# Kernel tuning notes

Hardware: AMD Instinct MI355X
Metric: run time of the kernel (lower is better)

## Reference

```python
import jax, jax.numpy as jnp
import numpy as np
import math

B, T, C = 1, 2048, 512
NH, NKV, HD, W = 8, 4, 64, 128  # heads, kv heads, head_dim, window_size
THETA = 10000.0
EPS = 1e-6


def _rms(x, w):
    # RMSNorm over last (head_dim) axis with learnable scale w
    return x * jax.lax.rsqrt(jnp.mean(x * x, axis=-1, keepdims=True) + EPS) * w


def _rope(x, cos, sin):
    # x: (B, H, T, HD); cos/sin: (T, HD//2). Half-split rotation.
    h = x.shape[-1] // 2
    x1, x2 = x[..., :h], x[..., h:]
    return jnp.concatenate([x1 * cos - x2 * sin, x2 * cos + x1 * sin], axis=-1)


def setup_inputs():
    key = jax.random.key(0)
    ks = jax.random.split(key, 5)
    x = jax.random.normal(ks[0], (B, T, C), jnp.float32)
    s = 1.0 / math.sqrt(C)
    W_q = jax.random.normal(ks[1], (C, NH * HD), jnp.float32) * s
    W_k = jax.random.normal(ks[2], (C, NKV * HD), jnp.float32) * s
    W_v = jax.random.normal(ks[3], (C, NKV * HD), jnp.float32) * s
    W_o = jax.random.normal(ks[4], (C, C), jnp.float32) * s
    q_norm_w = jnp.ones((HD,), jnp.float32)
    k_norm_w = jnp.ones((HD,), jnp.float32)
    pos = jnp.arange(T, dtype=jnp.float32)
    inv_freq = 1.0 / (THETA ** (jnp.arange(0, HD, 2, dtype=jnp.float32) / HD))
    ang = pos[:, None] * inv_freq[None, :]  # (T, HD//2)
    return {"x": x, "W_q": W_q, "W_k": W_k, "W_v": W_v, "W_o": W_o,
            "q_norm_w": q_norm_w, "k_norm_w": k_norm_w,
            "cos": jnp.cos(ang), "sin": jnp.sin(ang)}


def reference(x, W_q, W_k, W_v, W_o, q_norm_w, k_norm_w, cos, sin):
    q = (x @ W_q).reshape(B, T, NH, HD).transpose(0, 2, 1, 3)   # (B,NH,T,HD)
    k = (x @ W_k).reshape(B, T, NKV, HD).transpose(0, 2, 1, 3)  # (B,NKV,T,HD)
    v = (x @ W_v).reshape(B, T, NKV, HD).transpose(0, 2, 1, 3)
    q = _rope(q, cos, sin)
    k = _rope(k, cos, sin)
    q = _rms(q, q_norm_w)
    k = _rms(k, k_norm_w)
    g = NH // NKV  # GQA group size
    k = jnp.repeat(k, g, axis=1)  # (B,NH,T,HD)
    v = jnp.repeat(v, g, axis=1)
    # causal sliding-window: gather W-length windows ending at each position
    kp = jnp.pad(k, ((0, 0), (0, 0), (W - 1, 0), (0, 0)))
    vp = jnp.pad(v, ((0, 0), (0, 0), (W - 1, 0), (0, 0)))
    idx = jnp.arange(T)[:, None] + jnp.arange(W)[None, :]  # (T, W)
    kw = kp[:, :, idx, :]  # (B,NH,T,W,HD)
    vw = vp[:, :, idx, :]
    valid = jnp.arange(W)[None, :] >= (W - 1 - jnp.arange(T))[:, None]  # (T,W)
    attn = jnp.einsum('bhtd,bhtwd->bhtw', q, kw) / math.sqrt(HD)
    attn = jnp.where(valid[None, None], attn, -jnp.inf)
    attn = jax.nn.softmax(attn, axis=-1)
    out = jnp.einsum('bhtw,bhtwd->bhtd', attn, vw)  # (B,NH,T,HD)
    out = out.transpose(0, 2, 1, 3).reshape(B, T, C)
    return out @ W_o
```

## Files before the change

kernel.cpp:

```cpp
#include <hip/hip_runtime.h>
#include <hip/hip_bf16.h>
#include <math.h>

typedef float  f32x4  __attribute__((ext_vector_type(4)));
typedef short  s16x4  __attribute__((ext_vector_type(4)));
typedef short  s16x8  __attribute__((ext_vector_type(8)));
typedef unsigned short u16;

__device__ inline u16 f2b(float f) {
    __hip_bfloat16 h = __float2bfloat16(f);
    return *reinterpret_cast<u16*>(&h);
}
__device__ inline float b2f(u16 v) {
    return __uint_as_float(((unsigned)v) << 16);
}
__device__ inline void st_out(float* p, float v) { *p = v; }
__device__ inline void st_out(u16* p, float v)   { *p = f2b(v); }

__device__ inline void gload16(const void* g, void* l) {
    __builtin_amdgcn_global_load_lds(
        (const __attribute__((address_space(1))) void*)g,
        (__attribute__((address_space(3))) void*)l, 16, 0, 0);
}

__global__ __launch_bounds__(256) void prep(const float* __restrict__ x,
    const float* __restrict__ Wq, const float* __restrict__ Wk,
    const float* __restrict__ Wv, const float* __restrict__ Wo,
    u16* __restrict__ xb, u16* __restrict__ Wt, u16* __restrict__ Wot)
{
    const int tid = threadIdx.x, bid = blockIdx.x;
    if (bid >= 192) {
        int i = ((bid - 192) * 256 + tid) * 8;
        int row = i >> 9, col = i & 511;
        int scol = (col & ~63) | ((((col >> 3) & 7) ^ (row & 7)) << 3);
        float4 v0 = *(const float4*)(x + i);
        float4 v1 = *(const float4*)(x + i + 4);
        s16x8 o;
        o[0] = (short)f2b(v0.x); o[1] = (short)f2b(v0.y);
        o[2] = (short)f2b(v0.z); o[3] = (short)f2b(v0.w);
        o[4] = (short)f2b(v1.x); o[5] = (short)f2b(v1.y);
        o[6] = (short)f2b(v1.z); o[7] = (short)f2b(v1.w);
        *(s16x8*)(xb + (size_t)row * 512 + scol) = o;
        return;
    }
    __shared__ u16 Tsh[64][72];
    const float* src; u16* dst; int N, base, kt, nt;
    if (bid < 64)       { src = Wq; dst = Wt;  N = 512; base = 0;   kt = bid >> 3;       nt = bid & 7; }
    else if (bid < 96)  { src = Wk; dst = Wt;  N = 256; base = 512; kt = (bid-64) >> 2;  nt = (bid-64) & 3; }
    else if (bid < 128) { src = Wv; dst = Wt;  N = 256; base = 768; kt = (bid-96) >> 2;  nt = (bid-96) & 3; }
    else                { src = Wo; dst = Wot; N = 512; base = 0;   kt = (bid-128) >> 3; nt = (bid-128) & 7; }
    const int k0 = kt * 64, n0 = nt * 64;
    const int r = tid >> 2, c0 = (tid & 3) * 16;
#pragma unroll
    for (int j = 0; j < 4; ++j) {
        float4 v = *(const float4*)(src + (size_t)(k0 + r) * N + n0 + c0 + j * 4);
        Tsh[c0 + j*4 + 0][r] = f2b(v.x);
        Tsh[c0 + j*4 + 1][r] = f2b(v.y);
        Tsh[c0 + j*4 + 2][r] = f2b(v.z);
        Tsh[c0 + j*4 + 3][r] = f2b(v.w);
    }
    __syncthreads();
    const int n = tid >> 2, kc = (tid & 3) * 16;
    const int r7 = n & 7;
    const int cc0 = (kc >> 3) ^ r7;
    const int cc1 = ((kc >> 3) + 1) ^ r7;
    u16* oprow = dst + (size_t)(base + n0 + n) * 512 + k0;
    *(s16x8*)(oprow + cc0 * 8) = *(const s16x8*)&Tsh[n][kc];
    *(s16x8*)(oprow + cc1 * 8) = *(const s16x8*)&Tsh[n][kc + 8];
}

template<typename OutT>
__global__ __launch_bounds__(256) void gemm_mfma(const u16* __restrict__ A,
    const u16* __restrict__ Bt, OutT* __restrict__ C, int ldc)
{
    __shared__ u16 Ash[64][64];
    __shared__ u16 Bsh[64][64];
    const int tid = threadIdx.x;
    const int m0b = blockIdx.y * 64, n0b = blockIdx.x * 64;
    const int lane = tid & 63, wv = tid >> 6;
    const int q = lane & 15, g = lane >> 4;
    const int wm = (wv & 1) * 32, wn = (wv >> 1) * 32;
    const int lrow = lane >> 3, lchunk = lane & 7;
    const int s7 = q & 7;
    f32x4 acc[2][2] = {{{0,0,0,0},{0,0,0,0}},{{0,0,0,0},{0,0,0,0}}};
    for (int k0 = 0; k0 < 512; k0 += 64) {
        __syncthreads();
#pragma unroll
        for (int is = 0; is < 2; ++is) {
            const int rbase = is * 32 + wv * 8;
            gload16(A  + (size_t)(m0b + rbase + lrow) * 512 + k0 + lchunk * 8,
                    &Ash[rbase][0]);
            gload16(Bt + (size_t)(n0b + rbase + lrow) * 512 + k0 + lchunk * 8,
                    &Bsh[rbase][0]);
        }
        __syncthreads();
#pragma unroll
        for (int kk = 0; kk < 64; kk += 32) {
            const int cs = ((kk >> 3) + g) ^ s7;
            s16x8 af0 = *(const s16x8*)&Ash[wm + q][cs * 8];
            s16x8 af1 = *(const s16x8*)&Ash[wm + 16 + q][cs * 8];
            s16x8 bf0 = *(const s16x8*)&Bsh[wn + q][cs * 8];
            s16x8 bf1 = *(const s16x8*)&Bsh[wn + 16 + q][cs * 8];
            acc[0][0] = __builtin_amdgcn_mfma_f32_16x16x32_bf16(af0, bf0, acc[0][0], 0, 0, 0);
            acc[0][1] = __builtin_amdgcn_mfma_f32_16x16x32_bf16(af0, bf1, acc[0][1], 0, 0, 0);
            acc[1][0] = __builtin_amdgcn_mfma_f32_16x16x32_bf16(af1, bf0, acc[1][0], 0, 0, 0);
            acc[1][1] = __builtin_amdgcn_mfma_f32_16x16x32_bf16(af1, bf1, acc[1][1], 0, 0, 0);
        }
    }
#pragma unroll
    for (int mt = 0; mt < 2; ++mt)
#pragma unroll
        for (int nt = 0; nt < 2; ++nt)
#pragma unroll
            for (int r = 0; r < 4; ++r)
                st_out(&C[(size_t)(m0b + wm + mt*16 + g*4 + r) * ldc + n0b + wn + nt*16 + q],
                       acc[mt][nt][r]);
}

__global__ __launch_bounds__(256) void swa_mfma(const u16* __restrict__ qkvb,
    const float* __restrict__ cosT, const float* __restrict__ sinT,
    const float* __restrict__ qw, const float* __restrict__ kw,
    u16* __restrict__ attb)
{
    __shared__ u16 Ksh[160][72];
    __shared__ u16 Vt[64][162];
    const int tid = threadIdx.x;
    const int kvh = blockIdx.y;
    const int t0 = blockIdx.x * 32;
    for (int i = 0; i < 5; ++i) {
        int idx = i * 256 + tid;
        int j = idx >> 3, e = idx & 7, d0 = e * 8;
        int kt = t0 - 127 + j;
        if (kt < 0 || kt >= 2048) {
            s16x8 z = {0,0,0,0,0,0,0,0};
            *(s16x8*)&Ksh[j][d0] = z;
        } else {
            s16x8 raw = *(const s16x8*)(qkvb + (size_t)kt * 1024 + 512 + kvh * 64 + d0);
            float kv[8], ov[8];
#pragma unroll
            for (int ii = 0; ii < 8; ++ii) kv[ii] = b2f((u16)raw[ii]);
#pragma unroll
            for (int ii = 0; ii < 8; ++ii) ov[ii] = __shfl_xor(kv[ii], 4);
            const float* cp = cosT + kt * 32 + (e & 3) * 8;
            const float* sp = sinT + kt * 32 + (e & 3) * 8;
            float4 c0 = *(const float4*)(cp), c1 = *(const float4*)(cp + 4);
            float4 s0 = *(const float4*)(sp), s1 = *(const float4*)(sp + 4);
            float cf[8] = {c0.x,c0.y,c0.z,c0.w,c1.x,c1.y,c1.z,c1.w};
            float sf[8] = {s0.x,s0.y,s0.z,s0.w,s1.x,s1.y,s1.z,s1.w};
            const bool lo = (e < 4);
            float r[8]; float ssl = 0.f;
#pragma unroll
            for (int ii = 0; ii < 8; ++ii) {
                r[ii] = lo ? (kv[ii]*cf[ii] - ov[ii]*sf[ii])
                           : (kv[ii]*cf[ii] + ov[ii]*sf[ii]);
                ssl += r[ii] * r[ii];
            }
            ssl += __shfl_xor(ssl, 1);
            ssl += __shfl_xor(ssl, 2);
            ssl += __shfl_xor(ssl, 4);
            float scale = rsqrtf(ssl * (1.0f / 64.0f) + 1e-6f);
            float4 w0 = *(const float4*)(kw + d0), w1 = *(const float4*)(kw + d0 + 4);
            float wf[8] = {w0.x,w0.y,w0.z,w0.w,w1.x,w1.y,w1.z,w1.w};
            s16x8 outv;
#pragma unroll
            for (int ii = 0; ii < 8; ++ii) outv[ii] = (short)f2b(r[ii] * scale * wf[ii]);
            *(s16x8*)&Ksh[j][d0] = outv;
        }
    }
    for (int cch = 0; cch < 5; ++cch) {
        int w  = cch * 32 + (tid & 31);
        int d0 = (tid >> 5) * 8;
        int kt = t0 - 127 + w;
        s16x8 val = {0,0,0,0,0,0,0,0};
        if (kt >= 0 && kt < 2048)
            val = *(const s16x8*)(qkvb + (size_t)kt * 1024 + 768 + kvh * 64 + d0);
#pragma unroll
        for (int jj = 0; jj < 8; ++jj) Vt[d0 + jj][w] = ((const u16*)&val)[jj];
    }
    const int wv = tid >> 6, lane = tid & 63;
    const int q = lane & 15, g = lane >> 4;
    const int h  = 2 * kvh + (wv >> 1);
    const int tw = t0 + (wv & 1) * 16;
    const int jb = (wv & 1) * 16;
    const int t = tw + q;
    s16x8 qf0, qf1;
    {
        const u16* qp = qkvb + (size_t)t * 1024 + h * 64;
        s16x8 q0r = *(const s16x8*)(qp + g * 8);
        s16x8 q1r = *(const s16x8*)(qp + 32 + g * 8);
        const float* cp = cosT + t * 32 + g * 8;
        const float* sp = sinT + t * 32 + g * 8;
        float4 c0 = *(const float4*)(cp), c1 = *(const float4*)(cp + 4);
        float4 s0 = *(const float4*)(sp), s1 = *(const float4*)(sp + 4);
        float cf[8] = {c0.x,c0.y,c0.z,c0.w,c1.x,c1.y,c1.z,c1.w};
        float sf[8] = {s0.x,s0.y,s0.z,s0.w,s1.x,s1.y,s1.z,s1.w};
        float rl[8], rh[8]; float ssl = 0.f;
#pragma unroll
        for (int ii = 0; ii < 8; ++ii) {
            float ql = b2f((u16)q0r[ii]), qh = b2f((u16)q1r[ii]);
            rl[ii] = ql * cf[ii] - qh * sf[ii];
            rh[ii] = qh * cf[ii] + ql * sf[ii];
            ssl += rl[ii]*rl[ii] + rh[ii]*rh[ii];
        }
        ssl += __shfl_xor(ssl, 16);
        ssl += __shfl_xor(ssl, 32);
        float scale = rsqrtf(ssl * (1.0f / 64.0f) + 1e-6f);
        float4 wl0 = *(const float4*)(qw + g * 8), wl1 = *(const float4*)(qw + g * 8 + 4);
        float4 wh0 = *(const float4*)(qw + 32 + g * 8), wh1 = *(const float4*)(qw + 32 + g * 8 + 4);
        float wlo[8] = {wl0.x,wl0.y,wl0.z,wl0.w,wl1.x,wl1.y,wl1.z,wl1.w};
        float whi[8] = {wh0.x,wh0.y,wh0.z,wh0.w,wh1.x,wh1.y,wh1.z,wh1.w};
#pragma unroll
        for (int ii = 0; ii < 8; ++ii) {
            qf0[ii] = (short)f2b(rl[ii] * scale * wlo[ii]);
            qf1[ii] = (short)f2b(rh[ii] * scale * whi[ii]);
        }
    }
    __syncthreads();
    float s[9][4];
    float mx = -INFINITY;
    for (int wt = 0; wt < 9; ++wt) {
        int ldsrow = jb + wt * 16 + q;
        s16x8 kf0 = *(const s16x8*)&Ksh[ldsrow][g * 8];
        s16x8 kf1 = *(const s16x8*)&Ksh[ldsrow][32 + g * 8];
        f32x4 accv = {0, 0, 0, 0};
        accv = __builtin_amdgcn_mfma_f32_16x16x32_bf16(kf0, qf0, accv, 0, 0, 0);
        accv = __builtin_amdgcn_mfma_f32_16x16x32_bf16(kf1, qf1, accv, 0, 0, 0);
#pragma unroll
        for (int r = 0; r < 4; ++r) {
            int woff = wt * 16 + g * 4 + r;
            int key  = tw - 127 + woff;
            bool ok = (woff >= q) && (woff <= q + 127) && (key >= 0);
            float sv = ok ? accv[r] * 0.125f : -INFINITY;
            s[wt][r] = sv;
            mx = fmaxf(mx, sv);
        }
    }
    mx = fmaxf(mx, __shfl_xor(mx, 16));
    mx = fmaxf(mx, __shfl_xor(mx, 32));
    float sum = 0.f;
    s16x4 pb[9];
    for (int wt = 0; wt < 9; ++wt) {
#pragma unroll
        for (int r = 0; r < 4; ++r) {
            float p = __expf(s[wt][r] - mx);
            sum += p;
            pb[wt][r] = (short)f2b(p);
        }
    }
    sum += __shfl_xor(sum, 16);
    sum += __shfl_xor(sum, 32);
    float inv = 1.0f / sum;
    f32x4 oacc[4];
#pragma unroll
    for (int dt = 0; dt < 4; ++dt) {
        f32x4 a = {0, 0, 0, 0};
        for (int wt = 0; wt < 9; ++wt) {
            int col = jb + wt * 16 + g * 4;
            s16x4 vf = *(const s16x4*)&Vt[dt * 16 + q][col];
            a = __builtin_amdgcn_mfma_f32_16x16x16bf16_1k(vf, pb[wt], a, 0, 0, 0);
        }
        oacc[dt] = a;
    }
    __syncthreads();
    float (*Osh)[16][68] = (float (*)[16][68])&Ksh[0][0];
#pragma unroll
    for (int dt = 0; dt < 4; ++dt)
#pragma unroll
        for (int r = 0; r < 4; ++r)
            Osh[wv][q][dt * 16 + g * 4 + r] = oacc[dt][r] * inv;
    __syncthreads();
    const int qq = lane >> 2, dd0 = (lane & 3) * 16;
    const int r7 = qq & 7;
    u16* oprow = attb + (size_t)(tw + qq) * 512 + h * 64;
    s16x8 v0, v1;
#pragma unroll
    for (int j = 0; j < 8; ++j) v0[j] = (short)f2b(Osh[wv][qq][dd0 + j]);
#pragma unroll
    for (int j = 0; j < 8; ++j) v1[j] = (short)f2b(Osh[wv][qq][dd0 + 8 + j]);
    const int cc0 = (dd0 >> 3) ^ r7;
    const int cc1 = ((dd0 >> 3) + 1) ^ r7;
    *(s16x8*)(oprow + cc0 * 8) = v0;
    *(s16x8*)(oprow + cc1 * 8) = v1;
}

extern "C" void kernel_launch(void* const* d_in, const int* in_sizes, int n_in,
                              void* d_out, int out_size, void* d_ws, size_t ws_size,
                              hipStream_t stream)
{
    const float* x    = (const float*)d_in[0];
    const float* Wq   = (const float*)d_in[1];
    const float* Wk   = (const float*)d_in[2];
    const float* Wv   = (const float*)d_in[3];
    const float* Wo   = (const float*)d_in[4];
    const float* qw   = (const float*)d_in[5];
    const float* kw   = (const float*)d_in[6];
    const float* cosT = (const float*)d_in[7];
    const float* sinT = (const float*)d_in[8];

    u16* ws   = (u16*)d_ws;
    u16* xb   = ws;
    u16* Wt   = xb   + (size_t)2048 * 512;
    u16* Wot  = Wt   + (size_t)1024 * 512;
    u16* qkvb = Wot  + (size_t)512 * 512;
    u16* attb = qkvb + (size_t)2048 * 1024;

    dim3 blk(256);
    hipLaunchKernelGGL(prep, dim3(704), blk, 0, stream, x, Wq, Wk, Wv, Wo, xb, Wt, Wot);
    hipLaunchKernelGGL((gemm_mfma<u16>), dim3(16, 32), blk, 0, stream, xb, Wt, qkvb, 1024);
    hipLaunchKernelGGL(swa_mfma, dim3(64, 4), blk, 0, stream,
                       qkvb, cosT, sinT, qw, kw, attb);
    hipLaunchKernelGGL((gemm_mfma<float>), dim3(8, 32), blk, 0, stream,
                       attb, Wot, (float*)d_out, 512);
}
```

Baseline: 34.19 us.

## Double-buffer LDS tiles in MFMA GEMM to overlap global loads with compute

The GEMM kernel now keeps two LDS buffers per operand. It issues async global-to-LDS loads for the next K tile before computing on the current one, using explicit vmcnt waits and raw s_barrier calls in a fully unrolled 8-step loop. The goal is to hide global load latency that the old load-sync-compute-sync loop exposed. In exchange, LDS use per block doubles to 32KB, which may lower occupancy. It also relies on hand-written waitcnt counts being correct.

```diff
diff --git a/kernel.cpp b/kernel.cpp
--- a/kernel.cpp
+++ b/kernel.cpp
@@ -73,8 +73,8 @@
 __global__ __launch_bounds__(256) void gemm_mfma(const u16* __restrict__ A,
     const u16* __restrict__ Bt, OutT* __restrict__ C, int ldc)
 {
-    __shared__ u16 Ash[64][64];
-    __shared__ u16 Bsh[64][64];
+    __shared__ u16 Ash[2][64][64];
+    __shared__ u16 Bsh[2][64][64];
     const int tid = threadIdx.x;
     const int m0b = blockIdx.y * 64, n0b = blockIdx.x * 64;
     const int lane = tid & 63, wv = tid >> 6;
@@ -82,30 +82,46 @@
     const int wm = (wv & 1) * 32, wn = (wv >> 1) * 32;
     const int lrow = lane >> 3, lchunk = lane & 7;
     const int s7 = q & 7;
+    const int r0 = wv * 8, r1 = 32 + wv * 8;
     f32x4 acc[2][2] = {{{0,0,0,0},{0,0,0,0}},{{0,0,0,0},{0,0,0,0}}};
-    for (int k0 = 0; k0 < 512; k0 += 64) {
-        __syncthreads();
-#pragma unroll
-        for (int is = 0; is < 2; ++is) {
-            const int rbase = is * 32 + wv * 8;
-            gload16(A  + (size_t)(m0b + rbase + lrow) * 512 + k0 + lchunk * 8,
-                    &Ash[rbase][0]);
-            gload16(Bt + (size_t)(n0b + rbase + lrow) * 512 + k0 + lchunk * 8,
-                    &Bsh[rbase][0]);
-        }
-        __syncthreads();
+
+    {
+        gload16(A  + (size_t)(m0b + r0 + lrow) * 512 + lchunk * 8, &Ash[0][r0][0]);
+        gload16(Bt + (size_t)(n0b + r0 + lrow) * 512 + lchunk * 8, &Bsh[0][r0][0]);
+        gload16(A  + (size_t)(m0b + r1 + lrow) * 512 + lchunk * 8, &Ash[0][r1][0]);
+        gload16(Bt + (size_t)(n0b + r1 + lrow) * 512 + lchunk * 8, &Bsh[0][r1][0]);
+    }
+#pragma unroll
+    for (int it = 0; it < 8; ++it) {
+        const int cur = it & 1, nxt = cur ^ 1;
+        if (it < 7) {
+            const int k0 = (it + 1) * 64;
+            gload16(A  + (size_t)(m0b + r0 + lrow) * 512 + k0 + lchunk * 8, &Ash[nxt][r0][0]);
+            gload16(Bt + (size_t)(n0b + r0 + lrow) * 512 + k0 + lchunk * 8, &Bsh[nxt][r0][0]);
+            gload16(A  + (size_t)(m0b + r1 + lrow) * 512 + k0 + lchunk * 8, &Ash[nxt][r1][0]);
+            gload16(Bt + (size_t)(n0b + r1 + lrow) * 512 + k0 + lchunk * 8, &Bsh[nxt][r1][0]);
+            asm volatile("s_waitcnt vmcnt(4)" ::: "memory");
+        } else {
+            asm volatile("s_waitcnt vmcnt(0)" ::: "memory");
+        }
+        __builtin_amdgcn_sched_barrier(0);
+        __builtin_amdgcn_s_barrier();
+        __builtin_amdgcn_sched_barrier(0);
 #pragma unroll
         for (int kk = 0; kk < 64; kk += 32) {
             const int cs = ((kk >> 3) + g) ^ s7;
-            s16x8 af0 = *(const s16x8*)&Ash[wm + q][cs * 8];
-            s16x8 af1 = *(const s16x8*)&Ash[wm + 16 + q][cs * 8];
-            s16x8 bf0 = *(const s16x8*)&Bsh[wn + q][cs * 8];
-            s16x8 bf1 = *(const s16x8*)&Bsh[wn + 16 + q][cs * 8];
+            s16x8 af0 = *(const s16x8*)&Ash[cur][wm + q][cs * 8];
+            s16x8 af1 = *(const s16x8*)&Ash[cur][wm + 16 + q][cs * 8];
+            s16x8 bf0 = *(const s16x8*)&Bsh[cur][wn + q][cs * 8];
+            s16x8 bf1 = *(const s16x8*)&Bsh[cur][wn + 16 + q][cs * 8];
             acc[0][0] = __builtin_amdgcn_mfma_f32_16x16x32_bf16(af0, bf0, acc[0][0], 0, 0, 0);
             acc[0][1] = __builtin_amdgcn_mfma_f32_16x16x32_bf16(af0, bf1, acc[0][1], 0, 0, 0);
             acc[1][0] = __builtin_amdgcn_mfma_f32_16x16x32_bf16(af1, bf0, acc[1][0], 0, 0, 0);
             acc[1][1] = __builtin_amdgcn_mfma_f32_16x16x32_bf16(af1, bf1, acc[1][1], 0, 0, 0);
         }
+        __builtin_amdgcn_sched_barrier(0);
+        __builtin_amdgcn_s_barrier();
+        __builtin_amdgcn_sched_barrier(0);
     }
 #pragma unroll
     for (int mt = 0; mt < 2; ++mt)
```

After: 33.73 us. Within noise of the previous version (-1.4%).
